# Optimization experiments

Measured on AMD Instinct MI355X. Metric: run time of the kernel, lower is better.

Reference implementation:

```python
import jax, jax.numpy as jnp
import numpy as np

B, N, F_IN, F_OUT, H = 8, 1024, 256, 256, 4
HD = F_OUT // H  # head_dim = 64
NEG_SLOPE = 0.2


def setup_inputs() -> dict:
    key = jax.random.key(0)
    k1, k2, k3 = jax.random.split(key, 3)
    x = jax.random.normal(k1, (B, N, F_IN), dtype=jnp.float32)
    adj = jnp.ones((B, N, N), dtype=jnp.int32)
    # Linear weight, stored as [in, out] so h = x @ W
    W = jax.random.normal(k2, (F_IN, F_OUT), dtype=jnp.float32) / np.sqrt(F_IN)
    # attention vector a: [H, 2*head_dim], xavier-ish init
    a = jax.random.normal(k3, (H, 2 * HD), dtype=jnp.float32) * np.sqrt(2.0 / (H + 2 * HD))
    return {"x": x, "adj": adj, "W": W, "a": a}


def reference(x, adj, W, a):
    Bq, Nq, _ = x.shape
    h = (x @ W).reshape(Bq, Nq, H, HD).transpose(0, 2, 1, 3)  # [B,H,N,HD]
    a1, a2 = a[:, :HD], a[:, HD:]  # decompose concat: e_nm = h_n.a1 + h_m.a2
    s1 = jnp.einsum('bhnd,hd->bhn', h, a1)
    s2 = jnp.einsum('bhmd,hd->bhm', h, a2)
    e = jax.nn.leaky_relu(s1[:, :, :, None] + s2[:, :, None, :], NEG_SLOPE)  # [B,H,N,N]
    e = jnp.where(adj[:, None, :, :] == 0, -jnp.inf, e)
    attention = jax.nn.softmax(e, axis=-1)
    out = jnp.einsum('bhnm,bhmd->bhnd', attention, h)
    return out.transpose(0, 2, 1, 3).reshape(Bq, Nq, H * HD)
```

## Files before the change

kernel.cpp:

```cpp
#include <hip/hip_runtime.h>
#include <math.h>

#define H 4
#define HD 64
#define NN 1024
#define BB 8
#define FIN 256
#define FOUT 256

typedef _Float16 f16x8 __attribute__((ext_vector_type(8)));
typedef _Float16 f16x4 __attribute__((ext_vector_type(4)));
typedef _Float16 f16x2 __attribute__((ext_vector_type(2)));
typedef float f32x4 __attribute__((ext_vector_type(4)));

__global__ __launch_bounds__(256) void prep(const int* __restrict__ adj,
                                            unsigned* __restrict__ adjP,
                                            const float* __restrict__ W,
                                            _Float16* __restrict__ WT) {
  __shared__ float tile[64][68];
  const int tid = threadIdx.x;
  if (blockIdx.x < 1024) {
    size_t widx = (size_t)blockIdx.x * 256 + tid;
    const int4* p = (const int4*)adj + widx * 8;
    int4 v[8];
#pragma unroll
    for (int i = 0; i < 8; ++i) v[i] = p[i];
    unsigned bits = 0;
#pragma unroll
    for (int i = 0; i < 8; ++i) {
      bits |= (v[i].x != 0 ? 1u : 0u) << (4 * i);
      bits |= (v[i].y != 0 ? 2u : 0u) << (4 * i);
      bits |= (v[i].z != 0 ? 4u : 0u) << (4 * i);
      bits |= (v[i].w != 0 ? 8u : 0u) << (4 * i);
    }
    adjP[widx] = bits;
  } else {
    const int bx = blockIdx.x - 1024;
    const int k0 = (bx & 3) * 64, f0 = (bx >> 2) * 64;
    const int r = tid >> 4, c4 = (tid & 15) * 4;
#pragma unroll
    for (int p = 0; p < 4; ++p) {
      float4 v = *(const float4*)&W[(size_t)(k0 + p * 16 + r) * FOUT + f0 + c4];
      *(float4*)&tile[p * 16 + r][c4] = v;
    }
    __syncthreads();
    const int f = tid >> 2, kg = (tid & 3) * 16;
#pragma unroll
    for (int i = 0; i < 4; ++i) {
      f16x4 o;
#pragma unroll
      for (int j = 0; j < 4; ++j) o[j] = (_Float16)tile[kg + i * 4 + j][f];
      *(f16x4*)&WT[(size_t)(f0 + f) * FIN + k0 + kg + i * 4] = o;
    }
  }
}

__global__ __launch_bounds__(256) void gemm_xw(const float* __restrict__ x,
                                               const _Float16* __restrict__ WT,
                                               const float* __restrict__ a,
                                               _Float16* __restrict__ hT,
                                               float* __restrict__ s1_ws,
                                               float* __restrict__ s2_ws,
                                               float* __restrict__ u_ws,
                                               float* __restrict__ v_ws) {
  __shared__ _Float16 xs[64][264];
  const int tid = threadIdx.x;
  const int lane = tid & 63, w = tid >> 6;
  const int c = lane & 15, q = lane >> 4;
  const int bn0 = blockIdx.x * 64;
  const int head = blockIdx.y;
  const int b = bn0 >> 10, nb = bn0 & 1023;
  const int bh = b * H + head;

  float4 v[16];
#pragma unroll
  for (int p = 0; p < 16; ++p) {
    int f = p * 256 + tid;
    int row = f >> 6, col = (f & 63) * 4;
    v[p] = *(const float4*)&x[(size_t)(bn0 + row) * FIN + col];
  }
#pragma unroll
  for (int p = 0; p < 16; ++p) {
    int f = p * 256 + tid;
    int row = f >> 6, col = (f & 63) * 4;
    f16x4 h4;
    h4[0] = (_Float16)v[p].x; h4[1] = (_Float16)v[p].y;
    h4[2] = (_Float16)v[p].z; h4[3] = (_Float16)v[p].w;
    *(f16x4*)&xs[row][col] = h4;
  }
  __syncthreads();

  f32x4 acc[4];
#pragma unroll
  for (int t = 0; t < 4; ++t) acc[t] = (f32x4){0.f, 0.f, 0.f, 0.f};
  const _Float16* wbase = WT + (size_t)head * 64 * FIN;
#pragma unroll
  for (int ks = 0; ks < 8; ++ks) {
    f16x8 af = *(const f16x8*)&xs[w * 16 + c][ks * 32 + q * 8];
#pragma unroll
    for (int t = 0; t < 4; ++t) {
      f16x8 bf = *(const f16x8*)&wbase[(size_t)(t * 16 + c) * FIN + ks * 32 + q * 8];
      acc[t] = __builtin_amdgcn_mfma_f32_16x16x32_f16(af, bf, acc[t], 0, 0, 0);
    }
  }

  float a1v[4], a2v[4];
#pragma unroll
  for (int t = 0; t < 4; ++t) {
    a1v[t] = a[head * 2 * HD + t * 16 + c];
    a2v[t] = a[head * 2 * HD + HD + t * 16 + c];
  }
  float s1p[4] = {0.f, 0.f, 0.f, 0.f};
  float s2p[4] = {0.f, 0.f, 0.f, 0.f};
#pragma unroll
  for (int t = 0; t < 4; ++t) {
    f16x4 hv;
#pragma unroll
    for (int rr = 0; rr < 4; ++rr) {
      hv[rr] = (_Float16)acc[t][rr];
      s1p[rr] += acc[t][rr] * a1v[t];
      s2p[rr] += acc[t][rr] * a2v[t];
    }
    *(f16x4*)&hT[((size_t)(bh * 64 + t * 16 + c)) * NN + nb + w * 16 + q * 4] = hv;
  }
#pragma unroll
  for (int rr = 0; rr < 4; ++rr) {
    float s1 = s1p[rr], s2 = s2p[rr];
#pragma unroll
    for (int off = 8; off; off >>= 1) {
      s1 += __shfl_xor(s1, off);
      s2 += __shfl_xor(s2, off);
    }
    if (c == 0) {
      int n = nb + w * 16 + q * 4 + rr;
      size_t idx = (size_t)bh * NN + n;
      s1_ws[idx] = s1;
      s2_ws[idx] = s2;
      u_ws[idx] = __expf(s2);
      v_ws[idx] = __expf(0.2f * s2);
    }
  }
}

__global__ __launch_bounds__(256) void attn(const _Float16* __restrict__ hT,
                                            const float* __restrict__ s1_ws,
                                            const float* __restrict__ s2_ws,
                                            const float* __restrict__ u_ws,
                                            const float* __restrict__ v_ws,
                                            const unsigned* __restrict__ adjP,
                                            float* __restrict__ out) {
  __shared__ float s2r[NN], uu[NN], vv[NN];
  __shared__ _Float16 pt[2][32][136];
  __shared__ unsigned adjW[32][32];
  __shared__ float invL[32];
  const int tid = threadIdx.x, lane = tid & 63, w = tid >> 6;
  const int c = lane & 15, q = lane >> 4;
  const int ntile = blockIdx.x, bh = blockIdx.y;
  const int b = bh >> 2, head = bh & 3;
  const int n0 = ntile * 32;

  {
    size_t base = (size_t)bh * NN + tid * 4;
    *(float4*)&s2r[tid * 4] = *(const float4*)&s2_ws[base];
    *(float4*)&uu[tid * 4] = *(const float4*)&u_ws[base];
    *(float4*)&vv[tid * 4] = *(const float4*)&v_ws[base];
    uint4 aw = *(const uint4*)&adjP[((size_t)(b * NN + n0)) * 32 + tid * 4];
    *(uint4*)&adjW[tid >> 3][(tid * 4) & 31] = aw;
  }
  __syncthreads();

  float s1v[8];
#pragma unroll
  for (int r = 0; r < 8; ++r) s1v[r] = s1_ws[(size_t)bh * NN + n0 + w * 8 + r];

  const int wc = lane >> 4;
  const int shft = (2 * lane) & 31;

  float mx[8];
#pragma unroll
  for (int r = 0; r < 8; ++r) mx[r] = -INFINITY;
#pragma unroll
  for (int ch = 0; ch < 8; ++ch) {
    float2 s2p = *(const float2*)&s2r[ch * 128 + 2 * lane];
#pragma unroll
    for (int r = 0; r < 8; ++r) {
      unsigned bits = adjW[w * 8 + r][ch * 4 + wc] >> shft;
      mx[r] = fmaxf(mx[r], (bits & 1u) ? s2p.x : -INFINITY);
      mx[r] = fmaxf(mx[r], (bits & 2u) ? s2p.y : -INFINITY);
    }
  }
  float Arow[8], Brow[8], ns1[8];
#pragma unroll
  for (int r = 0; r < 8; ++r) {
    float m = mx[r];
#pragma unroll
    for (int off = 32; off; off >>= 1) m = fmaxf(m, __shfl_xor(m, off));
    float t0 = s1v[r] + m;
    float M = fmaxf(t0, 0.2f * t0);
    Arow[r] = __expf(s1v[r] - M);
    Brow[r] = __expf(0.2f * s1v[r] - M);
    ns1[r] = -s1v[r];
  }

  float Lp[8];
#pragma unroll
  for (int r = 0; r < 8; ++r) Lp[r] = 0.f;
  f32x4 acc[2];
  acc[0] = (f32x4){0.f, 0.f, 0.f, 0.f};
  acc[1] = (f32x4){0.f, 0.f, 0.f, 0.f};
  const _Float16* bptr = hT + ((size_t)bh * 64 + w * 16 + c) * NN + q * 8;

  f16x8 nbf0 = *(const f16x8*)(bptr);
  f16x8 nbf1 = *(const f16x8*)(bptr + 32);
  f16x8 nbf2 = *(const f16x8*)(bptr + 64);
  f16x8 nbf3 = *(const f16x8*)(bptr + 96);

  for (int ch = 0; ch < 8; ++ch) {
    const int buf = ch & 1;
    f16x8 bf0 = nbf0, bf1 = nbf1, bf2 = nbf2, bf3 = nbf3;
    float2 s2p = *(const float2*)&s2r[ch * 128 + 2 * lane];
    float2 up = *(const float2*)&uu[ch * 128 + 2 * lane];
    float2 vp = *(const float2*)&vv[ch * 128 + 2 * lane];
#pragma unroll
    for (int r = 0; r < 8; ++r) {
      unsigned bits = adjW[w * 8 + r][ch * 4 + wc] >> shft;
      float p0 = (s2p.x >= ns1[r]) ? Arow[r] * up.x : Brow[r] * vp.x;
      float p1 = (s2p.y >= ns1[r]) ? Arow[r] * up.y : Brow[r] * vp.y;
      p0 = (bits & 1u) ? p0 : 0.f;
      p1 = (bits & 2u) ? p1 : 0.f;
      Lp[r] += p0 + p1;
      f16x2 pk = __builtin_bit_cast(f16x2, __builtin_amdgcn_cvt_pkrtz(p0, p1));
      *(f16x2*)&pt[buf][w * 8 + r][2 * lane] = pk;
    }
    if (ch < 7) {
      nbf0 = *(const f16x8*)(bptr + (ch + 1) * 128);
      nbf1 = *(const f16x8*)(bptr + (ch + 1) * 128 + 32);
      nbf2 = *(const f16x8*)(bptr + (ch + 1) * 128 + 64);
      nbf3 = *(const f16x8*)(bptr + (ch + 1) * 128 + 96);
    }
    __syncthreads();
#pragma unroll
    for (int t = 0; t < 2; ++t) {
      f16x8 a0 = *(const f16x8*)&pt[buf][t * 16 + c][q * 8];
      f16x8 a1 = *(const f16x8*)&pt[buf][t * 16 + c][32 + q * 8];
      f16x8 a2 = *(const f16x8*)&pt[buf][t * 16 + c][64 + q * 8];
      f16x8 a3 = *(const f16x8*)&pt[buf][t * 16 + c][96 + q * 8];
      acc[t] = __builtin_amdgcn_mfma_f32_16x16x32_f16(a0, bf0, acc[t], 0, 0, 0);
      acc[t] = __builtin_amdgcn_mfma_f32_16x16x32_f16(a1, bf1, acc[t], 0, 0, 0);
      acc[t] = __builtin_amdgcn_mfma_f32_16x16x32_f16(a2, bf2, acc[t], 0, 0, 0);
      acc[t] = __builtin_amdgcn_mfma_f32_16x16x32_f16(a3, bf3, acc[t], 0, 0, 0);
    }
  }

  float myL = 0.f;
#pragma unroll
  for (int r = 0; r < 8; ++r) {
    float s = Lp[r];
#pragma unroll
    for (int off = 32; off; off >>= 1) s += __shfl_xor(s, off);
    if (lane == r) myL = s;
  }
  if (lane < 8) invL[w * 8 + lane] = 1.0f / myL;
  __syncthreads();
#pragma unroll
  for (int t = 0; t < 2; ++t) {
#pragma unroll
    for (int rr = 0; rr < 4; ++rr) {
      int nloc = t * 16 + q * 4 + rr;
      out[((size_t)(b * NN + n0 + nloc)) * FOUT + head * 64 + w * 16 + c] =
          acc[t][rr] * invL[nloc];
    }
  }
}

extern "C" void kernel_launch(void* const* d_in, const int* in_sizes, int n_in,
                              void* d_out, int out_size, void* d_ws, size_t ws_size,
                              hipStream_t stream) {
  const float* x = (const float*)d_in[0];
  const int* adj = (const int*)d_in[1];
  const float* W = (const float*)d_in[2];
  const float* a = (const float*)d_in[3];
  float* out = (float*)d_out;

  char* ws = (char*)d_ws;
  _Float16* hT = (_Float16*)ws;
  _Float16* WT = (_Float16*)(ws + (size_t)4 * 1024 * 1024);
  float* s1_ws = (float*)(ws + (size_t)4 * 1024 * 1024 + 128 * 1024);
  float* s2_ws = s1_ws + (size_t)BB * H * NN;
  float* u_ws = s2_ws + (size_t)BB * H * NN;
  float* v_ws = u_ws + (size_t)BB * H * NN;
  unsigned* adjP = (unsigned*)(v_ws + (size_t)BB * H * NN);

  prep<<<1040, 256, 0, stream>>>(adj, adjP, W, WT);
  gemm_xw<<<dim3(128, 4), 256, 0, stream>>>(x, WT, a, hT, s1_ws, s2_ws, u_ws, v_ws);
  attn<<<dim3(32, 32), 256, 0, stream>>>(hT, s1_ws, s2_ws, u_ws, v_ws, adjP, out);
}
```

Measured before the change: 119.1 us.

## Restructure attention so each wave owns rows and feeds P directly from registers

```diff
diff --git a/kernel.cpp b/kernel.cpp
--- a/kernel.cpp
+++ b/kernel.cpp
@@ -63,7 +63,7 @@
                                                float* __restrict__ s2_ws,
                                                float* __restrict__ u_ws,
                                                float* __restrict__ v_ws) {
-  __shared__ _Float16 xs[64][264];
+  __shared__ _Float16 wl[64][264];
   const int tid = threadIdx.x;
   const int lane = tid & 63, w = tid >> 6;
   const int c = lane & 15, q = lane >> 4;
@@ -72,34 +72,33 @@
   const int b = bn0 >> 10, nb = bn0 & 1023;
   const int bh = b * H + head;
 
-  float4 v[16];
-#pragma unroll
-  for (int p = 0; p < 16; ++p) {
-    int f = p * 256 + tid;
-    int row = f >> 6, col = (f & 63) * 4;
-    v[p] = *(const float4*)&x[(size_t)(bn0 + row) * FIN + col];
-  }
-#pragma unroll
-  for (int p = 0; p < 16; ++p) {
-    int f = p * 256 + tid;
-    int row = f >> 6, col = (f & 63) * 4;
-    f16x4 h4;
-    h4[0] = (_Float16)v[p].x; h4[1] = (_Float16)v[p].y;
-    h4[2] = (_Float16)v[p].z; h4[3] = (_Float16)v[p].w;
-    *(f16x4*)&xs[row][col] = h4;
+  {
+    const int row = tid >> 2, kseg = (tid & 3) * 64;
+    const _Float16* wp = WT + (size_t)(head * 64 + row) * FIN + kseg;
+#pragma unroll
+    for (int i = 0; i < 8; ++i) {
+      f16x8 t = *(const f16x8*)(wp + i * 8);
+      *(f16x8*)&wl[row][kseg + i * 8] = t;
+    }
   }
   __syncthreads();
 
   f32x4 acc[4];
 #pragma unroll
   for (int t = 0; t < 4; ++t) acc[t] = (f32x4){0.f, 0.f, 0.f, 0.f};
-  const _Float16* wbase = WT + (size_t)head * 64 * FIN;
+  const float* xp = x + (size_t)(bn0 + w * 16 + c) * FIN + q * 8;
 #pragma unroll
   for (int ks = 0; ks < 8; ++ks) {
-    f16x8 af = *(const f16x8*)&xs[w * 16 + c][ks * 32 + q * 8];
+    float4 xa = *(const float4*)(xp + ks * 32);
+    float4 xb = *(const float4*)(xp + ks * 32 + 4);
+    f16x8 af;
+    af[0] = (_Float16)xa.x; af[1] = (_Float16)xa.y;
+    af[2] = (_Float16)xa.z; af[3] = (_Float16)xa.w;
+    af[4] = (_Float16)xb.x; af[5] = (_Float16)xb.y;
+    af[6] = (_Float16)xb.z; af[7] = (_Float16)xb.w;
 #pragma unroll
     for (int t = 0; t < 4; ++t) {
-      f16x8 bf = *(const f16x8*)&wbase[(size_t)(t * 16 + c) * FIN + ks * 32 + q * 8];
+      f16x8 bf = *(const f16x8*)&wl[t * 16 + c][ks * 32 + q * 8];
       acc[t] = __builtin_amdgcn_mfma_f32_16x16x32_f16(af, bf, acc[t], 0, 0, 0);
     }
   }
@@ -150,125 +149,115 @@
                                             const unsigned* __restrict__ adjP,
                                             float* __restrict__ out) {
   __shared__ float s2r[NN], uu[NN], vv[NN];
-  __shared__ _Float16 pt[2][32][136];
-  __shared__ unsigned adjW[32][32];
-  __shared__ float invL[32];
-  const int tid = threadIdx.x, lane = tid & 63, w = tid >> 6;
+  __shared__ unsigned adjW[64][32];
+  const int tid = threadIdx.x, lane = tid & 63, wv = tid >> 6;
   const int c = lane & 15, q = lane >> 4;
   const int ntile = blockIdx.x, bh = blockIdx.y;
   const int b = bh >> 2, head = bh & 3;
-  const int n0 = ntile * 32;
+  const int n0 = ntile * 64;
+  const int myrow = wv * 16 + c;
 
   {
     size_t base = (size_t)bh * NN + tid * 4;
     *(float4*)&s2r[tid * 4] = *(const float4*)&s2_ws[base];
     *(float4*)&uu[tid * 4] = *(const float4*)&u_ws[base];
     *(float4*)&vv[tid * 4] = *(const float4*)&v_ws[base];
-    uint4 aw = *(const uint4*)&adjP[((size_t)(b * NN + n0)) * 32 + tid * 4];
-    *(uint4*)&adjW[tid >> 3][(tid * 4) & 31] = aw;
+    const int row = tid >> 2, wo = (tid & 3) * 8;
+    const uint4* ap = (const uint4*)(adjP + ((size_t)(b * NN + n0 + row)) * 32 + wo);
+    uint4 m0 = ap[0], m1 = ap[1];
+    *(uint4*)&adjW[row][wo] = m0;
+    *(uint4*)&adjW[row][wo + 4] = m1;
   }
   __syncthreads();
 
-  float s1v[8];
-#pragma unroll
-  for (int r = 0; r < 8; ++r) s1v[r] = s1_ws[(size_t)bh * NN + n0 + w * 8 + r];
-
-  const int wc = lane >> 4;
-  const int shft = (2 * lane) & 31;
-
-  float mx[8];
-#pragma unroll
-  for (int r = 0; r < 8; ++r) mx[r] = -INFINITY;
-#pragma unroll
-  for (int ch = 0; ch < 8; ++ch) {
-    float2 s2p = *(const float2*)&s2r[ch * 128 + 2 * lane];
-#pragma unroll
-    for (int r = 0; r < 8; ++r) {
-      unsigned bits = adjW[w * 8 + r][ch * 4 + wc] >> shft;
-      mx[r] = fmaxf(mx[r], (bits & 1u) ? s2p.x : -INFINITY);
-      mx[r] = fmaxf(mx[r], (bits & 2u) ? s2p.y : -INFINITY);
-    }
-  }
-  float Arow[8], Brow[8], ns1[8];
-#pragma unroll
-  for (int r = 0; r < 8; ++r) {
-    float m = mx[r];
-#pragma unroll
-    for (int off = 32; off; off >>= 1) m = fmaxf(m, __shfl_xor(m, off));
-    float t0 = s1v[r] + m;
-    float M = fmaxf(t0, 0.2f * t0);
-    Arow[r] = __expf(s1v[r] - M);
-    Brow[r] = __expf(0.2f * s1v[r] - M);
-    ns1[r] = -s1v[r];
-  }
-
-  float Lp[8];
-#pragma unroll
-  for (int r = 0; r < 8; ++r) Lp[r] = 0.f;
-  f32x4 acc[2];
-  acc[0] = (f32x4){0.f, 0.f, 0.f, 0.f};
-  acc[1] = (f32x4){0.f, 0.f, 0.f, 0.f};
-  const _Float16* bptr = hT + ((size_t)bh * 64 + w * 16 + c) * NN + q * 8;
-
-  f16x8 nbf0 = *(const f16x8*)(bptr);
-  f16x8 nbf1 = *(const f16x8*)(bptr + 32);
-  f16x8 nbf2 = *(const f16x8*)(bptr + 64);
-  f16x8 nbf3 = *(const f16x8*)(bptr + 96);
-
-  for (int ch = 0; ch < 8; ++ch) {
-    const int buf = ch & 1;
-    f16x8 bf0 = nbf0, bf1 = nbf1, bf2 = nbf2, bf3 = nbf3;
-    float2 s2p = *(const float2*)&s2r[ch * 128 + 2 * lane];
-    float2 up = *(const float2*)&uu[ch * 128 + 2 * lane];
-    float2 vp = *(const float2*)&vv[ch * 128 + 2 * lane];
-#pragma unroll
-    for (int r = 0; r < 8; ++r) {
-      unsigned bits = adjW[w * 8 + r][ch * 4 + wc] >> shft;
-      float p0 = (s2p.x >= ns1[r]) ? Arow[r] * up.x : Brow[r] * vp.x;
-      float p1 = (s2p.y >= ns1[r]) ? Arow[r] * up.y : Brow[r] * vp.y;
-      p0 = (bits & 1u) ? p0 : 0.f;
-      p1 = (bits & 2u) ? p1 : 0.f;
-      Lp[r] += p0 + p1;
-      f16x2 pk = __builtin_bit_cast(f16x2, __builtin_amdgcn_cvt_pkrtz(p0, p1));
-      *(f16x2*)&pt[buf][w * 8 + r][2 * lane] = pk;
-    }
-    if (ch < 7) {
-      nbf0 = *(const f16x8*)(bptr + (ch + 1) * 128);
-      nbf1 = *(const f16x8*)(bptr + (ch + 1) * 128 + 32);
-      nbf2 = *(const f16x8*)(bptr + (ch + 1) * 128 + 64);
-      nbf3 = *(const f16x8*)(bptr + (ch + 1) * 128 + 96);
-    }
-    __syncthreads();
-#pragma unroll
-    for (int t = 0; t < 2; ++t) {
-      f16x8 a0 = *(const f16x8*)&pt[buf][t * 16 + c][q * 8];
-      f16x8 a1 = *(const f16x8*)&pt[buf][t * 16 + c][32 + q * 8];
-      f16x8 a2 = *(const f16x8*)&pt[buf][t * 16 + c][64 + q * 8];
-      f16x8 a3 = *(const f16x8*)&pt[buf][t * 16 + c][96 + q * 8];
-      acc[t] = __builtin_amdgcn_mfma_f32_16x16x32_f16(a0, bf0, acc[t], 0, 0, 0);
-      acc[t] = __builtin_amdgcn_mfma_f32_16x16x32_f16(a1, bf1, acc[t], 0, 0, 0);
-      acc[t] = __builtin_amdgcn_mfma_f32_16x16x32_f16(a2, bf2, acc[t], 0, 0, 0);
-      acc[t] = __builtin_amdgcn_mfma_f32_16x16x32_f16(a3, bf3, acc[t], 0, 0, 0);
-    }
-  }
-
-  float myL = 0.f;
-#pragma unroll
-  for (int r = 0; r < 8; ++r) {
-    float s = Lp[r];
-#pragma unroll
-    for (int off = 32; off; off >>= 1) s += __shfl_xor(s, off);
-    if (lane == r) myL = s;
-  }
-  if (lane < 8) invL[w * 8 + lane] = 1.0f / myL;
-  __syncthreads();
-#pragma unroll
-  for (int t = 0; t < 2; ++t) {
+  const float s1 = s1_ws[(size_t)bh * NN + n0 + myrow];
+
+  float mx = -INFINITY;
+#pragma unroll 8
+  for (int kc = 0; kc < 32; ++kc) {
+    unsigned byte = (adjW[myrow][kc] >> (q * 8)) & 0xffu;
+    float4 sa = *(const float4*)&s2r[kc * 32 + q * 8];
+    float4 sb = *(const float4*)&s2r[kc * 32 + q * 8 + 4];
+    mx = fmaxf(mx, (byte & 1u) ? sa.x : -INFINITY);
+    mx = fmaxf(mx, (byte & 2u) ? sa.y : -INFINITY);
+    mx = fmaxf(mx, (byte & 4u) ? sa.z : -INFINITY);
+    mx = fmaxf(mx, (byte & 8u) ? sa.w : -INFINITY);
+    mx = fmaxf(mx, (byte & 16u) ? sb.x : -INFINITY);
+    mx = fmaxf(mx, (byte & 32u) ? sb.y : -INFINITY);
+    mx = fmaxf(mx, (byte & 64u) ? sb.z : -INFINITY);
+    mx = fmaxf(mx, (byte & 128u) ? sb.w : -INFINITY);
+  }
+  mx = fmaxf(mx, __shfl_xor(mx, 16));
+  mx = fmaxf(mx, __shfl_xor(mx, 32));
+  const float t0 = s1 + mx;
+  const float M = fmaxf(t0, 0.2f * t0);
+  const float Ar = __expf(s1 - M), Br = __expf(0.2f * s1 - M), ns1 = -s1;
+
+  f32x4 acc[4];
+#pragma unroll
+  for (int t = 0; t < 4; ++t) acc[t] = (f32x4){0.f, 0.f, 0.f, 0.f};
+  float psum = 0.f;
+  const _Float16* bp0 = hT + ((size_t)bh * 64 + c) * NN + q * 8;
+
+  f16x8 nbf[4];
+#pragma unroll
+  for (int t = 0; t < 4; ++t) nbf[t] = *(const f16x8*)(bp0 + (size_t)t * 16 * NN);
+
+#pragma unroll 4
+  for (int kc = 0; kc < 32; ++kc) {
+    f16x8 bf[4];
+#pragma unroll
+    for (int t = 0; t < 4; ++t) bf[t] = nbf[t];
+    unsigned byte = (adjW[myrow][kc] >> (q * 8)) & 0xffu;
+    float4 sa = *(const float4*)&s2r[kc * 32 + q * 8];
+    float4 sb = *(const float4*)&s2r[kc * 32 + q * 8 + 4];
+    float4 ua = *(const float4*)&uu[kc * 32 + q * 8];
+    float4 ub = *(const float4*)&uu[kc * 32 + q * 8 + 4];
+    float4 va = *(const float4*)&vv[kc * 32 + q * 8];
+    float4 vb = *(const float4*)&vv[kc * 32 + q * 8 + 4];
+    float p0 = (sa.x >= ns1) ? Ar * ua.x : Br * va.x;
+    float p1 = (sa.y >= ns1) ? Ar * ua.y : Br * va.y;
+    float p2 = (sa.z >= ns1) ? Ar * ua.z : Br * va.z;
+    float p3 = (sa.w >= ns1) ? Ar * ua.w : Br * va.w;
+    float p4 = (sb.x >= ns1) ? Ar * ub.x : Br * vb.x;
+    float p5 = (sb.y >= ns1) ? Ar * ub.y : Br * vb.y;
+    float p6 = (sb.z >= ns1) ? Ar * ub.z : Br * vb.z;
+    float p7 = (sb.w >= ns1) ? Ar * ub.w : Br * vb.w;
+    p0 = (byte & 1u) ? p0 : 0.f;
+    p1 = (byte & 2u) ? p1 : 0.f;
+    p2 = (byte & 4u) ? p2 : 0.f;
+    p3 = (byte & 8u) ? p3 : 0.f;
+    p4 = (byte & 16u) ? p4 : 0.f;
+    p5 = (byte & 32u) ? p5 : 0.f;
+    p6 = (byte & 64u) ? p6 : 0.f;
+    p7 = (byte & 128u) ? p7 : 0.f;
+    psum += ((p0 + p1) + (p2 + p3)) + ((p4 + p5) + (p6 + p7));
+    union { f16x8 v8; f16x2 v2[4]; } au;
+    au.v2[0] = __builtin_bit_cast(f16x2, __builtin_amdgcn_cvt_pkrtz(p0, p1));
+    au.v2[1] = __builtin_bit_cast(f16x2, __builtin_amdgcn_cvt_pkrtz(p2, p3));
+    au.v2[2] = __builtin_bit_cast(f16x2, __builtin_amdgcn_cvt_pkrtz(p4, p5));
+    au.v2[3] = __builtin_bit_cast(f16x2, __builtin_amdgcn_cvt_pkrtz(p6, p7));
+    if (kc < 31) {
+#pragma unroll
+      for (int t = 0; t < 4; ++t)
+        nbf[t] = *(const f16x8*)(bp0 + (size_t)t * 16 * NN + (kc + 1) * 32);
+    }
+#pragma unroll
+    for (int t = 0; t < 4; ++t)
+      acc[t] = __builtin_amdgcn_mfma_f32_16x16x32_f16(au.v8, bf[t], acc[t], 0, 0, 0);
+  }
+
+  psum += __shfl_xor(psum, 16);
+  psum += __shfl_xor(psum, 32);
+  float il[4];
+#pragma unroll
+  for (int rr = 0; rr < 4; ++rr) il[rr] = 1.0f / __shfl(psum, q * 4 + rr);
+#pragma unroll
+  for (int t = 0; t < 4; ++t) {
 #pragma unroll
     for (int rr = 0; rr < 4; ++rr) {
-      int nloc = t * 16 + q * 4 + rr;
-      out[((size_t)(b * NN + n0 + nloc)) * FOUT + head * 64 + w * 16 + c] =
-          acc[t][rr] * invL[nloc];
+      out[((size_t)(b * NN + n0 + wv * 16 + q * 4 + rr)) * FOUT + head * 64 + t * 16 + c] =
+          acc[t][rr] * il[rr];
     }
   }
 }
@@ -293,5 +282,5 @@
 
   prep<<<1040, 256, 0, stream>>>(adj, adjP, W, WT);
   gemm_xw<<<dim3(128, 4), 256, 0, stream>>>(x, WT, a, hT, s1_ws, s2_ws, u_ws, v_ws);
-  attn<<<dim3(32, 32), 256, 0, stream>>>(hT, s1_ws, s2_ws, u_ws, v_ws, adjP, out);
-}
+  attn<<<dim3(16, 32), 256, 0, stream>>>(hT, s1_ws, s2_ws, u_ws, v_ws, adjP, out);
+}
```

Result: slower. 131.6 us (+10.5%).
